# Optimization experiments

Measured on AMD Instinct MI355X. Metric: run time of the kernel, lower is better.

## Reference

```python
import jax, jax.numpy as jnp
import numpy as np

B = 1024      # total windows (batch*windows_per_image)
W = 7         # window_size
T = W * W     # tokens per window = 49
C = 256       # scaled_emb_dim = emb_dim * 2**level
H = 8         # heads
D = C // H    # head_dim = 32
NUM_POS = 2 * W - 1


def _relative_pos():
    coords = np.arange(W)
    coords = np.stack(np.meshgrid(coords, coords, indexing='ij')).reshape(2, -1)
    rp = coords[:, :, None] - coords[:, None, :] + (W - 1)
    return jnp.asarray(rp, dtype=jnp.int32)  # (2, T, T)


def setup_inputs() -> dict:
    key = jax.random.key(0)
    ks = jax.random.split(key, 12)
    s = 0.02
    return {
        'x': jax.random.normal(ks[0], (B, T, C), dtype=jnp.float32),
        'relative_pos': _relative_pos(),
        'bias_table': jax.random.truncated_normal(ks[1], -2.0, 2.0, (H, NUM_POS, NUM_POS), dtype=jnp.float32) * s,
        'wq': jax.random.normal(ks[2], (C, H, D), dtype=jnp.float32) / np.sqrt(C),
        'bq': jnp.zeros((H, D), dtype=jnp.float32),
        'wk': jax.random.normal(ks[3], (C, H, D), dtype=jnp.float32) / np.sqrt(C),
        'bk': jnp.zeros((H, D), dtype=jnp.float32),
        'wv': jax.random.normal(ks[4], (C, H, D), dtype=jnp.float32) / np.sqrt(C),
        'bv': jnp.zeros((H, D), dtype=jnp.float32),
        'wo': jax.random.normal(ks[5], (H, D, C), dtype=jnp.float32) / np.sqrt(C),
        'bo': jnp.zeros((C,), dtype=jnp.float32),
        'dw': jax.random.normal(ks[6], (C, C), dtype=jnp.float32) / np.sqrt(C),
        'db': jnp.zeros((C,), dtype=jnp.float32),
    }


def reference(x, relative_pos, bias_table, wq, bq, wk, bk, wv, bv, wo, bo, dw, db):
    # QKV projections (flax DenseGeneral with bias)
    q = jnp.einsum('btc,chd->bthd', x, wq) + bq  # (B,T,H,D)
    k = jnp.einsum('btc,chd->bthd', x, wk) + bk
    v = jnp.einsum('btc,chd->bthd', x, wv) + bv

    # gathered relative position bias: (H, T, T)
    bias = bias_table[:, relative_pos[0], relative_pos[1]]

    # attention logits with query scaling (flax dot_product_attention)
    q = q / jnp.sqrt(jnp.asarray(D, dtype=q.dtype))
    logits = jnp.einsum('bqhd,bkhd->bhqk', q, k) + bias[None]
    attn = jax.nn.softmax(logits, axis=-1)

    out = jnp.einsum('bhqk,bkhd->bqhd', attn, v)
    y = jnp.einsum('bqhd,hdc->bqc', out, wo) + bo  # attention out projection
    y = jnp.einsum('btc,cf->btf', y, dw) + db      # trailing Dense(scaled_emb_dim)
    return y
```

## Files before the change

kernel.cpp:

```cpp
#include <hip/hip_runtime.h>
#include <stdint.h>

#define T 49
#define CCH 256

typedef __bf16 bf16x8 __attribute__((ext_vector_type(8)));
typedef float f32x4 __attribute__((ext_vector_type(4)));

static __device__ __forceinline__ unsigned short f2bf(float f){
  uint32_t u = __builtin_bit_cast(uint32_t, f);
  u = u + 0x7fffu + ((u >> 16) & 1u);
  return (unsigned short)(u >> 16);
}
static __device__ __forceinline__ float bf2f(unsigned short h){
  return __builtin_bit_cast(float, ((uint32_t)h) << 16);
}
static __device__ __forceinline__ uint32_t pk2(float a, float b){
  return (uint32_t)f2bf(a) | ((uint32_t)f2bf(b) << 16);
}
static __device__ __forceinline__ f32x4 mfma16(bf16x8 a, bf16x8 b, f32x4 c){
  return __builtin_amdgcn_mfma_f32_16x16x32_bf16(a, b, c, 0, 0, 0);
}
#define SWZ(row) ((((row) & 7) << 4))

static __device__ __forceinline__ bf16x8 build_frag(uint32_t lo_w0, uint32_t lo_w1,
                                                    uint32_t hi_w0, uint32_t hi_w1,
                                                    int srcA, int srcB, bool use_hi){
  uint32_t a0 = (uint32_t)__shfl((int)lo_w0, srcA, 64);
  uint32_t c0 = (uint32_t)__shfl((int)hi_w0, srcA, 64);
  uint32_t a1 = (uint32_t)__shfl((int)lo_w1, srcA, 64);
  uint32_t c1 = (uint32_t)__shfl((int)hi_w1, srcA, 64);
  uint32_t a2 = (uint32_t)__shfl((int)lo_w0, srcB, 64);
  uint32_t c2 = (uint32_t)__shfl((int)hi_w0, srcB, 64);
  uint32_t a3 = (uint32_t)__shfl((int)lo_w1, srcB, 64);
  uint32_t c3 = (uint32_t)__shfl((int)hi_w1, srcB, 64);
  uint4 u = use_hi ? make_uint4(c0, c1, c2, c3) : make_uint4(a0, a1, a2, a3);
  return __builtin_bit_cast(bf16x8, u);
}


__global__ void prep_wqkvT(const float* __restrict__ wq, const float* __restrict__ wk,
                           const float* __restrict__ wv, unsigned short* __restrict__ out){
  int bk = blockIdx.x;
  int p = bk >> 8, kk = bk & 255;
  int n = threadIdx.x;
  const float* w = (p == 0) ? wq : (p == 1 ? wk : wv);
  float scl = (p == 0) ? 0.17677669529663687f : 1.0f;
  out[(size_t)(p * 256 + n) * 256 + kk] = f2bf(w[kk * 256 + n] * scl);
}

__global__ void prep_wodT(const float* __restrict__ wo, const float* __restrict__ dw,
                          unsigned short* __restrict__ out){
  int hd = blockIdx.x;
  int c = threadIdx.x;
  float s = 0.f;
  for (int cp = 0; cp < 256; ++cp) s = fmaf(wo[hd * 256 + cp], dw[cp * 256 + c], s);
  out[(size_t)c * 256 + hd] = f2bf(s);
}

__global__ void prep_misc(const int* __restrict__ rp, const float* __restrict__ btab,
                          const float* __restrict__ bq, const float* __restrict__ bk,
                          const float* __restrict__ bv, const float* __restrict__ bo,
                          const float* __restrict__ dwm, const float* __restrict__ db,
                          unsigned short* __restrict__ biasP, float* __restrict__ bqkv,
                          float* __restrict__ bod){
  int t = threadIdx.x;
  if (blockIdx.x == 0){
    for (int idx = t; idx < 768; idx += 256){
      int p = idx >> 8, n = idx & 255;
      float v = (p == 0) ? bq[n] * 0.17677669529663687f : (p == 1 ? bk[n] : bv[n]);
      bqkv[idx] = v;
    }
    float s = db[t];
    for (int cp = 0; cp < 256; ++cp) s = fmaf(bo[cp], dwm[cp * 256 + t], s);
    bod[t] = s;
  } else {
    int h = blockIdx.x - 1;
    for (int idx = t; idx < 4096; idx += 256){
      int r  = idx & 3;
      int lo = (idx >> 2) & 15;
      int g  = (idx >> 6) & 3;
      int nt = (idx >> 8) & 3;
      int jt = idx >> 10;
      int j = 16 * jt + 4 * g + r;
      int i = 16 * nt + lo;
      float v;
      if (j >= T) v = -1e30f;
      else if (i >= T) v = 0.f;
      else {
        int r0 = rp[i * 49 + j];
        int r1 = rp[2401 + i * 49 + j];
        v = btab[h * 169 + r0 * 13 + r1];
      }
      biasP[h * 4096 + idx] = f2bf(v);
    }
  }
}

__launch_bounds__(512, 4)
__global__ void wmsa_main(const float* __restrict__ x,
                          const unsigned short* __restrict__ wqkvT,
                          const unsigned short* __restrict__ wodT,
                          const unsigned short* __restrict__ biasP,
                          const float* __restrict__ bqkv,
                          const float* __restrict__ bod,
                          float* __restrict__ y){
  __shared__ unsigned short xs[64 * 256];

  const int b    = blockIdx.x;
  const int tid  = threadIdx.x;
  const int h    = tid >> 6;
  const int lane = tid & 63;
  const int g    = lane >> 4;
  const int lo   = lane & 15;
  char* xs_c = (char*)xs;

  const float* xb = x + (size_t)b * T * CCH;
  for (int idx = tid; idx < 64 * 64; idx += 512){
    int row = idx >> 6, c4 = idx & 63;
    float4 v = make_float4(0.f, 0.f, 0.f, 0.f);
    if (row < T) v = reinterpret_cast<const float4*>(xb)[row * 64 + c4];
    *reinterpret_cast<uint2*>(xs_c + row * 512 + ((c4 * 8) ^ SWZ(row)))
        = make_uint2(pk2(v.x, v.y), pk2(v.z, v.w));
  }
  __syncthreads();

  const int  srcA = lo + 16 * ((2 * g) & 3);
  const int  srcB = lo + 16 * ((2 * g + 1) & 3);
  const bool ghi  = (g >= 2);

  bf16x8 av[2][2];
  {
    f32x4 avc[4][2];
    #pragma unroll
    for (int mt = 0; mt < 4; ++mt)
      #pragma unroll
      for (int nt = 0; nt < 2; ++nt) avc[mt][nt] = f32x4{0,0,0,0};

    #pragma unroll 1
    for (int kt = 0; kt < 8; ++kt){
      bf16x8 ax[4];
      #pragma unroll
      for (int mt = 0; mt < 4; ++mt){
        int row = 16 * mt + lo;
        ax[mt] = *reinterpret_cast<const bf16x8*>(xs_c + row * 512 + ((kt * 64 + 16 * g) ^ SWZ(row)));
      }
      #pragma unroll
      for (int nt = 0; nt < 2; ++nt){
        const bf16x8 wvf = *reinterpret_cast<const bf16x8*>(
            wqkvT + (size_t)(512 + h * 32 + 16 * nt + lo) * 256 + kt * 32 + 8 * g);
        #pragma unroll
        for (int mt = 0; mt < 4; ++mt) avc[mt][nt] = mfma16(ax[mt], wvf, avc[mt][nt]);
      }
    }
    uint32_t pv[4][2][2];
    #pragma unroll
    for (int nt = 0; nt < 2; ++nt){
      const float bvs = bqkv[512 + h * 32 + 16 * nt + lo];
      #pragma unroll
      for (int mt = 0; mt < 4; ++mt){
        f32x4 tv = avc[mt][nt];
        tv[0] += bvs; tv[1] += bvs; tv[2] += bvs; tv[3] += bvs;
        pv[mt][nt][0] = pk2(tv[0], tv[1]); pv[mt][nt][1] = pk2(tv[2], tv[3]);
      }
    }
    #pragma unroll
    for (int dt = 0; dt < 2; ++dt)
      #pragma unroll
      for (int ktj = 0; ktj < 2; ++ktj)
        av[dt][ktj] = build_frag(pv[2 * ktj][dt][0], pv[2 * ktj][dt][1],
                                 pv[2 * ktj + 1][dt][0], pv[2 * ktj + 1][dt][1], srcA, srcB, ghi);
  }

  bf16x8 fk[4];
  {
    f32x4 akk[2][4];
    #pragma unroll
    for (int mt = 0; mt < 2; ++mt)
      #pragma unroll
      for (int nt = 0; nt < 4; ++nt) akk[mt][nt] = f32x4{0,0,0,0};

    #pragma unroll 1
    for (int kt = 0; kt < 8; ++kt){
      bf16x8 bx[4];
      #pragma unroll
      for (int nt = 0; nt < 4; ++nt){
        int row = 16 * nt + lo;
        bx[nt] = *reinterpret_cast<const bf16x8*>(xs_c + row * 512 + ((kt * 64 + 16 * g) ^ SWZ(row)));
      }
      #pragma unroll
      for (int mt = 0; mt < 2; ++mt){
        const bf16x8 wkf = *reinterpret_cast<const bf16x8*>(
            wqkvT + (size_t)(256 + h * 32 + 16 * mt + lo) * 256 + kt * 32 + 8 * g);
        #pragma unroll
        for (int nt = 0; nt < 4; ++nt) akk[mt][nt] = mfma16(wkf, bx[nt], akk[mt][nt]);
      }
    }
    uint32_t pkk[2][4][2];
    #pragma unroll
    for (int mt = 0; mt < 2; ++mt){
      const float4 b4k = *reinterpret_cast<const float4*>(bqkv + 256 + h * 32 + 16 * mt + 4 * g);
      #pragma unroll
      for (int nt = 0; nt < 4; ++nt){
        f32x4 tk = akk[mt][nt];
        tk[0] += b4k.x; tk[1] += b4k.y; tk[2] += b4k.z; tk[3] += b4k.w;
        pkk[mt][nt][0] = pk2(tk[0], tk[1]); pkk[mt][nt][1] = pk2(tk[2], tk[3]);
      }
    }
    #pragma unroll
    for (int nt = 0; nt < 4; ++nt)
      fk[nt] = build_frag(pkk[0][nt][0], pkk[0][nt][1], pkk[1][nt][0], pkk[1][nt][1], srcA, srcB, ghi);
  }

  bf16x8 fq[4];
  {
    f32x4 aq[2][4];
    #pragma unroll
    for (int mt = 0; mt < 2; ++mt)
      #pragma unroll
      for (int nt = 0; nt < 4; ++nt) aq[mt][nt] = f32x4{0,0,0,0};

    #pragma unroll 1
    for (int kt = 0; kt < 8; ++kt){
      bf16x8 bx[4];
      #pragma unroll
      for (int nt = 0; nt < 4; ++nt){
        int row = 16 * nt + lo;
        bx[nt] = *reinterpret_cast<const bf16x8*>(xs_c + row * 512 + ((kt * 64 + 16 * g) ^ SWZ(row)));
      }
      #pragma unroll
      for (int mt = 0; mt < 2; ++mt){
        const bf16x8 wqf = *reinterpret_cast<const bf16x8*>(
            wqkvT + (size_t)(h * 32 + 16 * mt + lo) * 256 + kt * 32 + 8 * g);
        #pragma unroll
        for (int nt = 0; nt < 4; ++nt) aq[mt][nt] = mfma16(wqf, bx[nt], aq[mt][nt]);
      }
    }
    uint32_t pq[2][4][2];
    #pragma unroll
    for (int mt = 0; mt < 2; ++mt){
      const float4 b4q = *reinterpret_cast<const float4*>(bqkv + h * 32 + 16 * mt + 4 * g);
      #pragma unroll
      for (int nt = 0; nt < 4; ++nt){
        f32x4 tq = aq[mt][nt];
        tq[0] += b4q.x; tq[1] += b4q.y; tq[2] += b4q.z; tq[3] += b4q.w;
        pq[mt][nt][0] = pk2(tq[0], tq[1]); pq[mt][nt][1] = pk2(tq[2], tq[3]);
      }
    }
    #pragma unroll
    for (int nt = 0; nt < 4; ++nt)
      fq[nt] = build_frag(pq[0][nt][0], pq[0][nt][1], pq[1][nt][0], pq[1][nt][1], srcA, srcB, ghi);
  }
  __syncthreads();

  #pragma unroll 1
  for (int nt = 0; nt < 4; ++nt){
    f32x4 lacc[4];
    #pragma unroll
    for (int jt = 0; jt < 4; ++jt){
      lacc[jt] = mfma16(fk[jt], fq[nt], f32x4{0,0,0,0});
      const uint2 bb = *reinterpret_cast<const uint2*>(
          biasP + h * 4096 + jt * 1024 + nt * 256 + (g * 16 + lo) * 4);
      lacc[jt][0] += bf2f((unsigned short)(bb.x & 0xffff));
      lacc[jt][1] += bf2f((unsigned short)(bb.x >> 16));
      lacc[jt][2] += bf2f((unsigned short)(bb.y & 0xffff));
      lacc[jt][3] += bf2f((unsigned short)(bb.y >> 16));
    }
    float m = -3.0e38f;
    #pragma unroll
    for (int jt = 0; jt < 4; ++jt)
      #pragma unroll
      for (int r = 0; r < 4; ++r) m = fmaxf(m, lacc[jt][r]);
    m = fmaxf(m, __shfl_xor(m, 16, 64));
    m = fmaxf(m, __shfl_xor(m, 32, 64));
    float ssum = 0.f;
    uint32_t pw[4][2];
    #pragma unroll
    for (int jt = 0; jt < 4; ++jt){
      f32x4 t = lacc[jt];
      #pragma unroll
      for (int r = 0; r < 4; ++r){
        t[r] = exp2f((t[r] - m) * 1.4426950408889634f);
        ssum += t[r];
      }
      pw[jt][0] = pk2(t[0], t[1]);
      pw[jt][1] = pk2(t[2], t[3]);
    }
    ssum += __shfl_xor(ssum, 16, 64);
    ssum += __shfl_xor(ssum, 32, 64);
    const float r0 = 1.f / ssum;

    bf16x8 pf0 = build_frag(pw[0][0], pw[0][1], pw[1][0], pw[1][1], srcA, srcB, ghi);
    bf16x8 pf1 = build_frag(pw[2][0], pw[2][1], pw[3][0], pw[3][1], srcA, srcB, ghi);

    const int i = 16 * nt + lo;
    #pragma unroll
    for (int dt = 0; dt < 2; ++dt){
      f32x4 oacc = mfma16(av[dt][0], pf0, f32x4{0,0,0,0});
      oacc = mfma16(av[dt][1], pf1, oacc);
      *reinterpret_cast<uint2*>(xs_c + i * 512 + ((h * 64 + dt * 32 + g * 8) ^ SWZ(i)))
          = make_uint2(pk2(oacc[0] * r0, oacc[1] * r0), pk2(oacc[2] * r0, oacc[3] * r0));
    }
  }
  __syncthreads();

  f32x4 facc[4][2];
  #pragma unroll
  for (int mt = 0; mt < 4; ++mt)
    #pragma unroll
    for (int nt = 0; nt < 2; ++nt) facc[mt][nt] = f32x4{0,0,0,0};

  #pragma unroll 1
  for (int kt = 0; kt < 8; ++kt){
    bf16x8 a[4];
    #pragma unroll
    for (int mt = 0; mt < 4; ++mt){
      int row = 16 * mt + lo;
      a[mt] = *reinterpret_cast<const bf16x8*>(xs_c + row * 512 + ((kt * 64 + 16 * g) ^ SWZ(row)));
    }
    #pragma unroll
    for (int nt = 0; nt < 2; ++nt){
      int crow = h * 32 + nt * 16 + lo;
      const bf16x8 bfr = *reinterpret_cast<const bf16x8*>(wodT + (size_t)crow * 256 + kt * 32 + 8 * g);
      #pragma unroll
      for (int mt = 0; mt < 4; ++mt) facc[mt][nt] = mfma16(a[mt], bfr, facc[mt][nt]);
    }
  }
  #pragma unroll
  for (int nt = 0; nt < 2; ++nt){
    int c = h * 32 + nt * 16 + lo;
    float bd = bod[c];
    #pragma unroll
    for (int mt = 0; mt < 4; ++mt)
      #pragma unroll
      for (int r = 0; r < 4; ++r){
        int i = 16 * mt + 4 * g + r;
        if (i < T) y[((size_t)b * T + i) * CCH + c] = facc[mt][nt][r] + bd;
      }
  }
}

extern "C" void kernel_launch(void* const* d_in, const int* in_sizes, int n_in,
                              void* d_out, int out_size, void* d_ws, size_t ws_size,
                              hipStream_t stream){
  const float* x    = (const float*)d_in[0];
  const int*   rp   = (const int*)d_in[1];
  const float* btab = (const float*)d_in[2];
  const float* wq   = (const float*)d_in[3];
  const float* bq   = (const float*)d_in[4];
  const float* wk   = (const float*)d_in[5];
  const float* bk   = (const float*)d_in[6];
  const float* wv   = (const float*)d_in[7];
  const float* bv   = (const float*)d_in[8];
  const float* wo   = (const float*)d_in[9];
  const float* bo   = (const float*)d_in[10];
  const float* dw   = (const float*)d_in[11];
  const float* db   = (const float*)d_in[12];
  float* y = (float*)d_out;

  char* ws = (char*)d_ws;
  unsigned short* wqkvT = (unsigned short*)(ws);
  unsigned short* wodT  = (unsigned short*)(ws + 393216);
  unsigned short* biasP = (unsigned short*)(ws + 524288);
  float* bqkv           = (float*)(ws + 589824);
  float* bod            = (float*)(ws + 592896);

  prep_wqkvT<<<768, 256, 0, stream>>>(wq, wk, wv, wqkvT);
  prep_wodT<<<256, 256, 0, stream>>>(wo, dw, wodT);
  prep_misc<<<9, 256, 0, stream>>>(rp, btab, bq, bk, bv, bo, dw, db, biasP, bqkv, bod);
  wmsa_main<<<1024, 512, 0, stream>>>(x, wqkvT, wodT, biasP, bqkv, bod, y);
}
```

Before: 144.0 us.

## Split fused window-attention kernel into bf16 prep, per-head attention, and output GEMM

Unfuses the monolithic per-window kernel into three stages. A pre-pass converts x to a padded bf16 buffer in global memory. A per-(window, head) wavefront kernel with no shared memory computes QKV and attention and writes bf16 attention outputs to global. A separate token-tiled GEMM then applies the fused out-projection weight. The aim is to remove the LDS staging and block-wide syncs and to raise occupancy with smaller blocks. In exchange it adds roughly 50MB of extra global traffic plus two extra launches, and each wave re-reads x from global/L2 three times.

```diff
diff --git a/kernel.cpp b/kernel.cpp
--- a/kernel.cpp
+++ b/kernel.cpp
@@ -8,9 +8,8 @@
 typedef float f32x4 __attribute__((ext_vector_type(4)));
 
 static __device__ __forceinline__ unsigned short f2bf(float f){
-  uint32_t u = __builtin_bit_cast(uint32_t, f);
-  u = u + 0x7fffu + ((u >> 16) & 1u);
-  return (unsigned short)(u >> 16);
+  __bf16 h = (__bf16)f;
+  return __builtin_bit_cast(unsigned short, h);
 }
 static __device__ __forceinline__ float bf2f(unsigned short h){
   return __builtin_bit_cast(float, ((uint32_t)h) << 16);
@@ -21,7 +20,6 @@
 static __device__ __forceinline__ f32x4 mfma16(bf16x8 a, bf16x8 b, f32x4 c){
   return __builtin_amdgcn_mfma_f32_16x16x32_bf16(a, b, c, 0, 0, 0);
 }
-#define SWZ(row) ((((row) & 7) << 4))
 
 static __device__ __forceinline__ bf16x8 build_frag(uint32_t lo_w0, uint32_t lo_w1,
                                                     uint32_t hi_w0, uint32_t hi_w1,
@@ -38,6 +36,23 @@
   return __builtin_bit_cast(bf16x8, u);
 }
 
+
+__global__ void prep_xbf(const float* __restrict__ x, unsigned short* __restrict__ xg){
+  const unsigned int NV = 50176u * 256u / 8u;
+  const unsigned int NT = 50240u * 256u / 8u;
+  for (unsigned int idx = blockIdx.x * blockDim.x + threadIdx.x; idx < NT;
+       idx += gridDim.x * blockDim.x){
+    uint4 o;
+    if (idx < NV){
+      const float4 a = reinterpret_cast<const float4*>(x)[(size_t)idx * 2];
+      const float4 c = reinterpret_cast<const float4*>(x)[(size_t)idx * 2 + 1];
+      o = make_uint4(pk2(a.x, a.y), pk2(a.z, a.w), pk2(c.x, c.y), pk2(c.z, c.w));
+    } else {
+      o = make_uint4(0u, 0u, 0u, 0u);
+    }
+    reinterpret_cast<uint4*>(xg)[idx] = o;
+  }
+}
 
 __global__ void prep_wqkvT(const float* __restrict__ wq, const float* __restrict__ wk,
                            const float* __restrict__ wv, unsigned short* __restrict__ out){
@@ -97,61 +112,58 @@
   }
 }
 
-__launch_bounds__(512, 4)
-__global__ void wmsa_main(const float* __restrict__ x,
-                          const unsigned short* __restrict__ wqkvT,
-                          const unsigned short* __restrict__ wodT,
-                          const unsigned short* __restrict__ biasP,
-                          const float* __restrict__ bqkv,
-                          const float* __restrict__ bod,
-                          float* __restrict__ y){
-  __shared__ unsigned short xs[64 * 256];
-
-  const int b    = blockIdx.x;
+__launch_bounds__(256, 4)
+__global__ void qkv_attn(const unsigned short* __restrict__ xg,
+                         const unsigned short* __restrict__ wqkvT,
+                         const float* __restrict__ bqkv,
+                         const unsigned short* __restrict__ biasP,
+                         unsigned short* __restrict__ og){
   const int tid  = threadIdx.x;
-  const int h    = tid >> 6;
+  const int wv_  = tid >> 6;
   const int lane = tid & 63;
   const int g    = lane >> 4;
   const int lo   = lane & 15;
-  char* xs_c = (char*)xs;
-
-  const float* xb = x + (size_t)b * T * CCH;
-  for (int idx = tid; idx < 64 * 64; idx += 512){
-    int row = idx >> 6, c4 = idx & 63;
-    float4 v = make_float4(0.f, 0.f, 0.f, 0.f);
-    if (row < T) v = reinterpret_cast<const float4*>(xb)[row * 64 + c4];
-    *reinterpret_cast<uint2*>(xs_c + row * 512 + ((c4 * 8) ^ SWZ(row)))
-        = make_uint2(pk2(v.x, v.y), pk2(v.z, v.w));
-  }
-  __syncthreads();
+  const int task = blockIdx.x * 4 + wv_;
+  const int b    = task >> 3;
+  const int h    = task & 7;
 
   const int  srcA = lo + 16 * ((2 * g) & 3);
   const int  srcB = lo + 16 * ((2 * g + 1) & 3);
   const bool ghi  = (g >= 2);
 
-  bf16x8 av[2][2];
+  const unsigned short* xw = xg + (size_t)b * 49 * 256;
+
+  bf16x8 av[2][2], fk[4], fq[4];
+
   {
-    f32x4 avc[4][2];
+    f32x4 acc[4][2];
     #pragma unroll
     for (int mt = 0; mt < 4; ++mt)
       #pragma unroll
-      for (int nt = 0; nt < 2; ++nt) avc[mt][nt] = f32x4{0,0,0,0};
+      for (int nt = 0; nt < 2; ++nt) acc[mt][nt] = f32x4{0,0,0,0};
 
     #pragma unroll 1
-    for (int kt = 0; kt < 8; ++kt){
-      bf16x8 ax[4];
-      #pragma unroll
-      for (int mt = 0; mt < 4; ++mt){
-        int row = 16 * mt + lo;
-        ax[mt] = *reinterpret_cast<const bf16x8*>(xs_c + row * 512 + ((kt * 64 + 16 * g) ^ SWZ(row)));
-      }
-      #pragma unroll
-      for (int nt = 0; nt < 2; ++nt){
-        const bf16x8 wvf = *reinterpret_cast<const bf16x8*>(
-            wqkvT + (size_t)(512 + h * 32 + 16 * nt + lo) * 256 + kt * 32 + 8 * g);
-        #pragma unroll
-        for (int mt = 0; mt < 4; ++mt) avc[mt][nt] = mfma16(ax[mt], wvf, avc[mt][nt]);
-      }
+    for (int kb = 0; kb < 4; ++kb){
+      bf16x8 xf[2][4], wf[2][2];
+      #pragma unroll
+      for (int q2 = 0; q2 < 2; ++q2){
+        const int kt = kb * 2 + q2;
+        #pragma unroll
+        for (int mt = 0; mt < 4; ++mt)
+          xf[q2][mt] = *reinterpret_cast<const bf16x8*>(
+              xw + (size_t)(16 * mt + lo) * 256 + kt * 32 + 8 * g);
+        #pragma unroll
+        for (int nt = 0; nt < 2; ++nt)
+          wf[q2][nt] = *reinterpret_cast<const bf16x8*>(
+              wqkvT + (size_t)(512 + h * 32 + 16 * nt + lo) * 256 + kt * 32 + 8 * g);
+      }
+      #pragma unroll
+      for (int q2 = 0; q2 < 2; ++q2)
+        #pragma unroll
+        for (int nt = 0; nt < 2; ++nt)
+          #pragma unroll
+          for (int mt = 0; mt < 4; ++mt)
+            acc[mt][nt] = mfma16(xf[q2][mt], wf[q2][nt], acc[mt][nt]);
     }
     uint32_t pv[4][2][2];
     #pragma unroll
@@ -159,9 +171,9 @@
       const float bvs = bqkv[512 + h * 32 + 16 * nt + lo];
       #pragma unroll
       for (int mt = 0; mt < 4; ++mt){
-        f32x4 tv = avc[mt][nt];
-        tv[0] += bvs; tv[1] += bvs; tv[2] += bvs; tv[3] += bvs;
-        pv[mt][nt][0] = pk2(tv[0], tv[1]); pv[mt][nt][1] = pk2(tv[2], tv[3]);
+        f32x4 t = acc[mt][nt];
+        t[0] += bvs; t[1] += bvs; t[2] += bvs; t[3] += bvs;
+        pv[mt][nt][0] = pk2(t[0], t[1]); pv[mt][nt][1] = pk2(t[2], t[3]);
       }
     }
     #pragma unroll
@@ -169,108 +181,125 @@
       #pragma unroll
       for (int ktj = 0; ktj < 2; ++ktj)
         av[dt][ktj] = build_frag(pv[2 * ktj][dt][0], pv[2 * ktj][dt][1],
-                                 pv[2 * ktj + 1][dt][0], pv[2 * ktj + 1][dt][1], srcA, srcB, ghi);
-  }
-
-  bf16x8 fk[4];
+                                 pv[2 * ktj + 1][dt][0], pv[2 * ktj + 1][dt][1],
+                                 srcA, srcB, ghi);
+  }
+
   {
-    f32x4 akk[2][4];
+    f32x4 acc[2][4];
     #pragma unroll
     for (int mt = 0; mt < 2; ++mt)
       #pragma unroll
-      for (int nt = 0; nt < 4; ++nt) akk[mt][nt] = f32x4{0,0,0,0};
+      for (int nt = 0; nt < 4; ++nt) acc[mt][nt] = f32x4{0,0,0,0};
 
     #pragma unroll 1
-    for (int kt = 0; kt < 8; ++kt){
-      bf16x8 bx[4];
+    for (int kb = 0; kb < 4; ++kb){
+      bf16x8 xf[2][4], wf[2][2];
+      #pragma unroll
+      for (int q2 = 0; q2 < 2; ++q2){
+        const int kt = kb * 2 + q2;
+        #pragma unroll
+        for (int nt = 0; nt < 4; ++nt)
+          xf[q2][nt] = *reinterpret_cast<const bf16x8*>(
+              xw + (size_t)(16 * nt + lo) * 256 + kt * 32 + 8 * g);
+        #pragma unroll
+        for (int mt = 0; mt < 2; ++mt)
+          wf[q2][mt] = *reinterpret_cast<const bf16x8*>(
+              wqkvT + (size_t)(256 + h * 32 + 16 * mt + lo) * 256 + kt * 32 + 8 * g);
+      }
+      #pragma unroll
+      for (int q2 = 0; q2 < 2; ++q2)
+        #pragma unroll
+        for (int mt = 0; mt < 2; ++mt)
+          #pragma unroll
+          for (int nt = 0; nt < 4; ++nt)
+            acc[mt][nt] = mfma16(wf[q2][mt], xf[q2][nt], acc[mt][nt]);
+    }
+    uint32_t pkk[2][4][2];
+    #pragma unroll
+    for (int mt = 0; mt < 2; ++mt){
+      const float4 b4 = *reinterpret_cast<const float4*>(bqkv + 256 + h * 32 + 16 * mt + 4 * g);
       #pragma unroll
       for (int nt = 0; nt < 4; ++nt){
-        int row = 16 * nt + lo;
-        bx[nt] = *reinterpret_cast<const bf16x8*>(xs_c + row * 512 + ((kt * 64 + 16 * g) ^ SWZ(row)));
-      }
-      #pragma unroll
-      for (int mt = 0; mt < 2; ++mt){
-        const bf16x8 wkf = *reinterpret_cast<const bf16x8*>(
-            wqkvT + (size_t)(256 + h * 32 + 16 * mt + lo) * 256 + kt * 32 + 8 * g);
-        #pragma unroll
-        for (int nt = 0; nt < 4; ++nt) akk[mt][nt] = mfma16(wkf, bx[nt], akk[mt][nt]);
-      }
-    }
-    uint32_t pkk[2][4][2];
+        f32x4 t = acc[mt][nt];
+        t[0] += b4.x; t[1] += b4.y; t[2] += b4.z; t[3] += b4.w;
+        pkk[mt][nt][0] = pk2(t[0], t[1]); pkk[mt][nt][1] = pk2(t[2], t[3]);
+      }
+    }
+    #pragma unroll
+    for (int nt = 0; nt < 4; ++nt)
+      fk[nt] = build_frag(pkk[0][nt][0], pkk[0][nt][1], pkk[1][nt][0], pkk[1][nt][1],
+                          srcA, srcB, ghi);
+  }
+
+  {
+    f32x4 acc[2][4];
+    #pragma unroll
+    for (int mt = 0; mt < 2; ++mt)
+      #pragma unroll
+      for (int nt = 0; nt < 4; ++nt) acc[mt][nt] = f32x4{0,0,0,0};
+
+    #pragma unroll 1
+    for (int kb = 0; kb < 4; ++kb){
+      bf16x8 xf[2][4], wf[2][2];
+      #pragma unroll
+      for (int q2 = 0; q2 < 2; ++q2){
+        const int kt = kb * 2 + q2;
+        #pragma unroll
+        for (int nt = 0; nt < 4; ++nt)
+          xf[q2][nt] = *reinterpret_cast<const bf16x8*>(
+              xw + (size_t)(16 * nt + lo) * 256 + kt * 32 + 8 * g);
+        #pragma unroll
+        for (int mt = 0; mt < 2; ++mt)
+          wf[q2][mt] = *reinterpret_cast<const bf16x8*>(
+              wqkvT + (size_t)(h * 32 + 16 * mt + lo) * 256 + kt * 32 + 8 * g);
+      }
+      #pragma unroll
+      for (int q2 = 0; q2 < 2; ++q2)
+        #pragma unroll
+        for (int mt = 0; mt < 2; ++mt)
+          #pragma unroll
+          for (int nt = 0; nt < 4; ++nt)
+            acc[mt][nt] = mfma16(wf[q2][mt], xf[q2][nt], acc[mt][nt]);
+    }
+    uint32_t pq[2][4][2];
     #pragma unroll
     for (int mt = 0; mt < 2; ++mt){
-      const float4 b4k = *reinterpret_cast<const float4*>(bqkv + 256 + h * 32 + 16 * mt + 4 * g);
+      const float4 b4 = *reinterpret_cast<const float4*>(bqkv + h * 32 + 16 * mt + 4 * g);
       #pragma unroll
       for (int nt = 0; nt < 4; ++nt){
-        f32x4 tk = akk[mt][nt];
-        tk[0] += b4k.x; tk[1] += b4k.y; tk[2] += b4k.z; tk[3] += b4k.w;
-        pkk[mt][nt][0] = pk2(tk[0], tk[1]); pkk[mt][nt][1] = pk2(tk[2], tk[3]);
+        f32x4 t = acc[mt][nt];
+        t[0] += b4.x; t[1] += b4.y; t[2] += b4.z; t[3] += b4.w;
+        pq[mt][nt][0] = pk2(t[0], t[1]); pq[mt][nt][1] = pk2(t[2], t[3]);
       }
     }
     #pragma unroll
     for (int nt = 0; nt < 4; ++nt)
-      fk[nt] = build_frag(pkk[0][nt][0], pkk[0][nt][1], pkk[1][nt][0], pkk[1][nt][1], srcA, srcB, ghi);
-  }
-
-  bf16x8 fq[4];
-  {
-    f32x4 aq[2][4];
-    #pragma unroll
-    for (int mt = 0; mt < 2; ++mt)
-      #pragma unroll
-      for (int nt = 0; nt < 4; ++nt) aq[mt][nt] = f32x4{0,0,0,0};
-
-    #pragma unroll 1
-    for (int kt = 0; kt < 8; ++kt){
-      bf16x8 bx[4];
-      #pragma unroll
-      for (int nt = 0; nt < 4; ++nt){
-        int row = 16 * nt + lo;
-        bx[nt] = *reinterpret_cast<const bf16x8*>(xs_c + row * 512 + ((kt * 64 + 16 * g) ^ SWZ(row)));
-      }
-      #pragma unroll
-      for (int mt = 0; mt < 2; ++mt){
-        const bf16x8 wqf = *reinterpret_cast<const bf16x8*>(
-            wqkvT + (size_t)(h * 32 + 16 * mt + lo) * 256 + kt * 32 + 8 * g);
-        #pragma unroll
-        for (int nt = 0; nt < 4; ++nt) aq[mt][nt] = mfma16(wqf, bx[nt], aq[mt][nt]);
-      }
-    }
-    uint32_t pq[2][4][2];
-    #pragma unroll
-    for (int mt = 0; mt < 2; ++mt){
-      const float4 b4q = *reinterpret_cast<const float4*>(bqkv + h * 32 + 16 * mt + 4 * g);
-      #pragma unroll
-      for (int nt = 0; nt < 4; ++nt){
-        f32x4 tq = aq[mt][nt];
-        tq[0] += b4q.x; tq[1] += b4q.y; tq[2] += b4q.z; tq[3] += b4q.w;
-        pq[mt][nt][0] = pk2(tq[0], tq[1]); pq[mt][nt][1] = pk2(tq[2], tq[3]);
-      }
-    }
-    #pragma unroll
-    for (int nt = 0; nt < 4; ++nt)
-      fq[nt] = build_frag(pq[0][nt][0], pq[0][nt][1], pq[1][nt][0], pq[1][nt][1], srcA, srcB, ghi);
-  }
-  __syncthreads();
+      fq[nt] = build_frag(pq[0][nt][0], pq[0][nt][1], pq[1][nt][0], pq[1][nt][1],
+                          srcA, srcB, ghi);
+  }
 
   #pragma unroll 1
   for (int nt = 0; nt < 4; ++nt){
+    uint2 bb[4];
+    #pragma unroll
+    for (int jt = 0; jt < 4; ++jt)
+      bb[jt] = *reinterpret_cast<const uint2*>(
+          biasP + h * 4096 + jt * 1024 + nt * 256 + (g * 16 + lo) * 4);
     f32x4 lacc[4];
     #pragma unroll
     for (int jt = 0; jt < 4; ++jt){
       lacc[jt] = mfma16(fk[jt], fq[nt], f32x4{0,0,0,0});
-      const uint2 bb = *reinterpret_cast<const uint2*>(
-          biasP + h * 4096 + jt * 1024 + nt * 256 + (g * 16 + lo) * 4);
-      lacc[jt][0] += bf2f((unsigned short)(bb.x & 0xffff));
-      lacc[jt][1] += bf2f((unsigned short)(bb.x >> 16));
-      lacc[jt][2] += bf2f((unsigned short)(bb.y & 0xffff));
-      lacc[jt][3] += bf2f((unsigned short)(bb.y >> 16));
-    }
-    float m = -3.0e38f;
-    #pragma unroll
-    for (int jt = 0; jt < 4; ++jt)
-      #pragma unroll
-      for (int r = 0; r < 4; ++r) m = fmaxf(m, lacc[jt][r]);
+      lacc[jt][0] += bf2f((unsigned short)(bb[jt].x & 0xffff));
+      lacc[jt][1] += bf2f((unsigned short)(bb[jt].x >> 16));
+      lacc[jt][2] += bf2f((unsigned short)(bb[jt].y & 0xffff));
+      lacc[jt][3] += bf2f((unsigned short)(bb[jt].y >> 16));
+    }
+    float m01a = fmaxf(fmaxf(lacc[0][0], lacc[0][1]), fmaxf(lacc[0][2], lacc[0][3]));
+    float m01b = fmaxf(fmaxf(lacc[1][0], lacc[1][1]), fmaxf(lacc[1][2], lacc[1][3]));
+    float m23a = fmaxf(fmaxf(lacc[2][0], lacc[2][1]), fmaxf(lacc[2][2], lacc[2][3]));
+    float m23b = fmaxf(fmaxf(lacc[3][0], lacc[3][1]), fmaxf(lacc[3][2], lacc[3][3]));
+    float m = fmaxf(fmaxf(m01a, m01b), fmaxf(m23a, m23b));
     m = fmaxf(m, __shfl_xor(m, 16, 64));
     m = fmaxf(m, __shfl_xor(m, 32, 64));
     float ssum = 0.f;
@@ -298,45 +327,62 @@
     for (int dt = 0; dt < 2; ++dt){
       f32x4 oacc = mfma16(av[dt][0], pf0, f32x4{0,0,0,0});
       oacc = mfma16(av[dt][1], pf1, oacc);
-      *reinterpret_cast<uint2*>(xs_c + i * 512 + ((h * 64 + dt * 32 + g * 8) ^ SWZ(i)))
-          = make_uint2(pk2(oacc[0] * r0, oacc[1] * r0), pk2(oacc[2] * r0, oacc[3] * r0));
-    }
-  }
-  __syncthreads();
-
-  f32x4 facc[4][2];
+      if (i < T)
+        *reinterpret_cast<uint2*>(og + ((size_t)b * T + i) * 256 + h * 32 + 16 * dt + 4 * g)
+            = make_uint2(pk2(oacc[0] * r0, oacc[1] * r0), pk2(oacc[2] * r0, oacc[3] * r0));
+    }
+  }
+}
+
+__launch_bounds__(512, 4)
+__global__ void out_c(const unsigned short* __restrict__ og,
+                      const unsigned short* __restrict__ wodT,
+                      const float* __restrict__ bod,
+                      float* __restrict__ y){
+  const int tid  = threadIdx.x;
+  const int w    = tid >> 6;
+  const int lane = tid & 63;
+  const int g    = lane >> 4;
+  const int lo   = lane & 15;
+  const int tok0 = blockIdx.x * 64;
+
+  f32x4 acc[2][4];
   #pragma unroll
-  for (int mt = 0; mt < 4; ++mt)
-    #pragma unroll
-    for (int nt = 0; nt < 2; ++nt) facc[mt][nt] = f32x4{0,0,0,0};
-
-  #pragma unroll 1
+  for (int mt = 0; mt < 2; ++mt)
+    #pragma unroll
+    for (int nt = 0; nt < 4; ++nt) acc[mt][nt] = f32x4{0,0,0,0};
+
+  #pragma unroll 2
   for (int kt = 0; kt < 8; ++kt){
-    bf16x8 a[4];
-    #pragma unroll
-    for (int mt = 0; mt < 4; ++mt){
-      int row = 16 * mt + lo;
-      a[mt] = *reinterpret_cast<const bf16x8*>(xs_c + row * 512 + ((kt * 64 + 16 * g) ^ SWZ(row)));
-    }
-    #pragma unroll
-    for (int nt = 0; nt < 2; ++nt){
-      int crow = h * 32 + nt * 16 + lo;
-      const bf16x8 bfr = *reinterpret_cast<const bf16x8*>(wodT + (size_t)crow * 256 + kt * 32 + 8 * g);
-      #pragma unroll
-      for (int mt = 0; mt < 4; ++mt) facc[mt][nt] = mfma16(a[mt], bfr, facc[mt][nt]);
-    }
-  }
+    bf16x8 aw[2], bo_[4];
+    #pragma unroll
+    for (int mt = 0; mt < 2; ++mt)
+      aw[mt] = *reinterpret_cast<const bf16x8*>(
+          wodT + (size_t)(32 * w + 16 * mt + lo) * 256 + kt * 32 + 8 * g);
+    #pragma unroll
+    for (int nt = 0; nt < 4; ++nt)
+      bo_[nt] = *reinterpret_cast<const bf16x8*>(
+          og + (size_t)(tok0 + 16 * nt + lo) * 256 + kt * 32 + 8 * g);
+    #pragma unroll
+    for (int mt = 0; mt < 2; ++mt)
+      #pragma unroll
+      for (int nt = 0; nt < 4; ++nt) acc[mt][nt] = mfma16(aw[mt], bo_[nt], acc[mt][nt]);
+  }
+
   #pragma unroll
-  for (int nt = 0; nt < 2; ++nt){
-    int c = h * 32 + nt * 16 + lo;
-    float bd = bod[c];
-    #pragma unroll
-    for (int mt = 0; mt < 4; ++mt)
-      #pragma unroll
-      for (int r = 0; r < 4; ++r){
-        int i = 16 * mt + 4 * g + r;
-        if (i < T) y[((size_t)b * T + i) * CCH + c] = facc[mt][nt][r] + bd;
-      }
+  for (int mt = 0; mt < 2; ++mt){
+    const int cb = 32 * w + 16 * mt + 4 * g;
+    const float4 b4 = *reinterpret_cast<const float4*>(bod + cb);
+    #pragma unroll
+    for (int nt = 0; nt < 4; ++nt){
+      const int tok = tok0 + 16 * nt + lo;
+      float4 o;
+      o.x = acc[mt][nt][0] + b4.x;
+      o.y = acc[mt][nt][1] + b4.y;
+      o.z = acc[mt][nt][2] + b4.z;
+      o.w = acc[mt][nt][3] + b4.w;
+      *reinterpret_cast<float4*>(y + (size_t)tok * 256 + cb) = o;
+    }
   }
 }
 
@@ -359,14 +405,22 @@
   float* y = (float*)d_out;
 
   char* ws = (char*)d_ws;
-  unsigned short* wqkvT = (unsigned short*)(ws);
-  unsigned short* wodT  = (unsigned short*)(ws + 393216);
-  unsigned short* biasP = (unsigned short*)(ws + 524288);
-  float* bqkv           = (float*)(ws + 589824);
-  float* bod            = (float*)(ws + 592896);
-
+  const size_t XG_BYTES = 25722880ull;
+  const size_t OG_BYTES = 25690112ull;
+
+  unsigned short* xg = (unsigned short*)(ws);
+  unsigned short* og = (unsigned short*)(ws + XG_BYTES);
+  char* wsp = ws + XG_BYTES + OG_BYTES;
+  unsigned short* wqkvT = (unsigned short*)(wsp);
+  unsigned short* wodT  = (unsigned short*)(wsp + 393216);
+  unsigned short* biasP = (unsigned short*)(wsp + 524288);
+  float* bqkv           = (float*)(wsp + 589824);
+  float* bod            = (float*)(wsp + 592896);
+
+  prep_xbf<<<2048, 256, 0, stream>>>(x, xg);
   prep_wqkvT<<<768, 256, 0, stream>>>(wq, wk, wv, wqkvT);
   prep_wodT<<<256, 256, 0, stream>>>(wo, dw, wodT);
   prep_misc<<<9, 256, 0, stream>>>(rp, btab, bq, bk, bv, bo, dw, db, biasP, bqkv, bod);
-  wmsa_main<<<1024, 512, 0, stream>>>(x, wqkvT, wodT, biasP, bqkv, bod, y);
-}
+  qkv_attn<<<2048, 256, 0, stream>>>(xg, wqkvT, bqkv, biasP, og);
+  out_c<<<784, 512, 0, stream>>>(og, wodT, bod, y);
+}
```

Result: slower. 244.1 us (+69.5%).
